# Optimization experiments

Hardware: AMD Instinct MI355X
Metric: run time of the kernel (lower is better)

The kernel has to match this reference:

```python
import jax, jax.numpy as jnp
import numpy as np

N, S, E = 8, 1024, 768
H = 12
D = E // H  # head_dim = 64
FF = 4 * E
EPS = 1e-5


def setup_inputs() -> dict:
    key = jax.random.key(0)
    ks = jax.random.split(key, 12)
    s = lambda fan_in: 1.0 / np.sqrt(fan_in)
    return {
        "x": jax.random.normal(ks[0], (N, S, E), dtype=jnp.float32),
        "ln1_g": jnp.ones((E,), jnp.float32),
        "ln1_b": jnp.zeros((E,), jnp.float32),
        "ln2_g": jnp.ones((E,), jnp.float32),
        "ln2_b": jnp.zeros((E,), jnp.float32),
        "w_attn": jax.random.normal(ks[1], (E, 3 * E), jnp.float32) * s(E),
        "b_attn": jax.random.normal(ks[2], (3 * E,), jnp.float32) * 0.02,
        "w_proj": jax.random.normal(ks[3], (E, E), jnp.float32) * s(E),
        "b_proj": jax.random.normal(ks[4], (E,), jnp.float32) * 0.02,
        "w_fc": jax.random.normal(ks[5], (E, FF), jnp.float32) * s(E),
        "b_fc": jax.random.normal(ks[6], (FF,), jnp.float32) * 0.02,
        "w_fc2": jax.random.normal(ks[7], (FF, E), jnp.float32) * s(FF),
        "b_fc2": jax.random.normal(ks[8], (E,), jnp.float32) * 0.02,
    }


def _layernorm(x, g, b):
    mu = jnp.mean(x, axis=-1, keepdims=True)
    var = jnp.var(x, axis=-1, keepdims=True)
    return (x - mu) * jax.lax.rsqrt(var + EPS) * g + b


def reference(x, ln1_g, ln1_b, ln2_g, ln2_b, w_attn, b_attn, w_proj, b_proj,
              w_fc, b_fc, w_fc2, b_fc2):
    # --- attention branch (pre-LN) ---
    h = _layernorm(x, ln1_g, ln1_b)
    qkv = h @ w_attn + b_attn                       # [N,S,3E]
    q, k, v = jnp.split(qkv, 3, axis=-1)
    q = q.reshape(N, S, H, D).transpose(0, 2, 1, 3)  # [N,H,S,D]
    k = k.reshape(N, S, H, D).transpose(0, 2, 1, 3)
    v = v.reshape(N, S, H, D).transpose(0, 2, 1, 3)
    attn = jnp.einsum('nhsd,nhtd->nhst', q, k) * (1.0 / np.sqrt(D))
    causal = jnp.tril(jnp.ones((S, S), bool))
    attn = jnp.where(causal, attn, -jnp.inf)
    p = jax.nn.softmax(attn, axis=-1)
    out = jnp.einsum('nhst,nhtd->nhsd', p, v)        # [N,H,S,D]
    out = out.transpose(0, 2, 1, 3).reshape(N, S, E)
    x = x + (out @ w_proj + b_proj)
    # --- MLP branch ---
    h2 = _layernorm(x, ln2_g, ln2_b)
    ff = jax.nn.gelu(h2 @ w_fc + b_fc, approximate=False)  # exact GELU (torch nn.GELU default)
    x = x + (ff @ w_fc2 + b_fc2)
    return x
```

## Files before the change

kernel.cpp:

```cpp
#include <hip/hip_runtime.h>
#include <hip/hip_bf16.h>
#include <stdint.h>

#define S_LEN 1024
#define E_DIM 768
#define H_N   12
#define FF_DIM 3072

typedef __hip_bfloat16 bf16;
using short8  = __attribute__((ext_vector_type(8))) short;
using short4v = __attribute__((ext_vector_type(4))) short;
using f32x4   = __attribute__((ext_vector_type(4))) float;

__device__ __forceinline__ void async_cp16(const void* g, void* l) {
  __builtin_amdgcn_global_load_lds(
      (__attribute__((address_space(1))) void*)(g),
      (__attribute__((address_space(3))) void*)(l), 16, 0, 0);
}

__global__ __launch_bounds__(256) void wcastT(const float* __restrict__ w,
                                              bf16* __restrict__ wt,
                                              int K, int N) {
  __shared__ float t[32][33];
  int bx = blockIdx.x;
  int by = blockIdx.y;
  int x = threadIdx.x & 31;
  int y = threadIdx.x >> 5;
  for (int i = y; i < 32; i += 8)
    t[i][x] = w[(size_t)(by * 32 + i) * N + bx * 32 + x];
  __syncthreads();
  for (int i = y; i < 32; i += 8)
    wt[(size_t)(bx * 32 + i) * K + by * 32 + x] = __float2bfloat16(t[x][i]);
}

__global__ __launch_bounds__(256) void ln_rows(const float* __restrict__ x,
                                               const float* __restrict__ g,
                                               const float* __restrict__ b,
                                               bf16* __restrict__ out) {
  int row = blockIdx.x;
  int tid = threadIdx.x;
  const float* xr = x + (size_t)row * E_DIM;
  float v0 = xr[tid], v1 = xr[tid + 256], v2 = xr[tid + 512];
  float s = v0 + v1 + v2;
  float ss = v0 * v0 + v1 * v1 + v2 * v2;
  for (int o = 32; o > 0; o >>= 1) {
    s  += __shfl_down(s, o);
    ss += __shfl_down(ss, o);
  }
  __shared__ float ps[4], pq[4];
  int wv = tid >> 6;
  if ((tid & 63) == 0) { ps[wv] = s; pq[wv] = ss; }
  __syncthreads();
  s  = ps[0] + ps[1] + ps[2] + ps[3];
  ss = pq[0] + pq[1] + pq[2] + pq[3];
  float mu  = s * (1.0f / E_DIM);
  float var = ss * (1.0f / E_DIM) - mu * mu;
  float rs  = rsqrtf(var + 1e-5f);
  bf16* orow = out + (size_t)row * E_DIM;
  orow[tid]       = __float2bfloat16((v0 - mu) * rs * g[tid]       + b[tid]);
  orow[tid + 256] = __float2bfloat16((v1 - mu) * rs * g[tid + 256] + b[tid + 256]);
  orow[tid + 512] = __float2bfloat16((v2 - mu) * rs * g[tid + 512] + b[tid + 512]);
}

template <int MODE>
__global__ __launch_bounds__(256) void gemm_bt(
    const bf16* __restrict__ A, const bf16* __restrict__ Bt,
    const float* __restrict__ bias, const float* __restrict__ resid,
    float* __restrict__ outf, bf16* __restrict__ ob0, bf16* __restrict__ ob1,
    bf16* __restrict__ ob2, int M, int N, int K) {
  __shared__ bf16 As[2][128 * 64];
  __shared__ bf16 Bs[2][128 * 64];
  int tid = threadIdx.x;
  int wave = tid >> 6, lane = tid & 63;
  int quad = lane >> 4, l16 = lane & 15;
  int gx = N >> 7;
  int flat = blockIdx.x;
  int y8 = flat & 7;
  int q2 = flat >> 3;
  int bx = q2 % gx;
  int by = (q2 / gx) * 8 + y8;
  int m0 = by * 128, n0 = bx * 128;
  int wm = (wave & 1) * 64, wn = (wave >> 1) * 64;
  f32x4 acc[4][4];
  for (int i = 0; i < 4; i++)
    for (int j = 0; j < 4; j++)
      for (int r = 0; r < 4; r++) acc[i][j][r] = 0.f;

  int xs = l16 & 7;
  int srow = tid >> 3;
  int cg = (((tid & 7) ^ (srow & 7)) << 3);
  const bf16* aptr = A  + (size_t)(m0 + srow) * K + cg;
  const bf16* bptr = Bt + (size_t)(n0 + srow) * K + cg;

  int nkb = K >> 6;
  {
    bf16* la = &As[0][0] + tid * 8;
    bf16* lb = &Bs[0][0] + tid * 8;
#pragma unroll
    for (int t = 0; t < 4; ++t) {
      async_cp16(aptr + (size_t)t * 32 * K, la + t * 2048);
      async_cp16(bptr + (size_t)t * 32 * K, lb + t * 2048);
    }
  }
  for (int ik = 0; ik < nkb; ++ik) {
    int cur = ik & 1;
    __syncthreads();
    short8 af[2][4], bfr[2][4];
#pragma unroll
    for (int ks = 0; ks < 2; ks++) {
      int ko = (((ks * 4 + quad) ^ xs) << 3);
      for (int i = 0; i < 4; i++)
        af[ks][i] = *(const short8*)&As[cur][(wm + i * 16 + l16) * 64 + ko];
      for (int j = 0; j < 4; j++)
        bfr[ks][j] = *(const short8*)&Bs[cur][(wn + j * 16 + l16) * 64 + ko];
    }
    if (ik + 1 < nkb) {
      size_t ko = (size_t)(ik + 1) * 64;
      bf16* la = &As[cur ^ 1][0] + tid * 8;
      bf16* lb = &Bs[cur ^ 1][0] + tid * 8;
#pragma unroll
      for (int t = 0; t < 4; ++t) {
        async_cp16(aptr + ko + (size_t)t * 32 * K, la + t * 2048);
        async_cp16(bptr + ko + (size_t)t * 32 * K, lb + t * 2048);
      }
    }
#pragma unroll
    for (int ks = 0; ks < 2; ks++)
      for (int i = 0; i < 4; i++)
        for (int j = 0; j < 4; j++)
          acc[i][j] = __builtin_amdgcn_mfma_f32_16x16x32_bf16(
              bfr[ks][j], af[ks][i], acc[i][j], 0, 0, 0);
  }

  for (int j = 0; j < 4; j++) {
    int colb = n0 + wn + j * 16 + quad * 4;
    f32x4 b4 = *(const f32x4*)&bias[colb];
    for (int i = 0; i < 4; i++) {
      int row = m0 + wm + i * 16 + l16;
      f32x4 v = acc[i][j] + b4;
      if (MODE == 0) {
        int nn = row >> 10, s = row & 1023;
        if (colb < 768) {
          int h = colb >> 6, db = colb & 63;
          short4v pk;
          for (int r = 0; r < 4; r++)
            pk[r] = __builtin_bit_cast(short, __float2bfloat16(v[r] * 0.125f));
          *(short4v*)&ob0[(((size_t)nn * H_N + h) * S_LEN + s) * 64 + db] = pk;
        } else if (colb < 1536) {
          int c = colb - 768;
          size_t nh2 = (size_t)nn * H_N + (c >> 6);
          int d = c & 63;
          short4v pk;
          for (int r = 0; r < 4; r++)
            pk[r] = __builtin_bit_cast(short, __float2bfloat16(v[r]));
          *(short4v*)&ob1[((nh2 * 8 + (d >> 3)) * S_LEN + s) * 8 + (d & 7)] = pk;
        } else {
          int c = colb - 1536;
          size_t nh2 = (size_t)nn * H_N + (c >> 6);
          int d0 = c & 63;
          for (int r = 0; r < 4; r++)
            ob2[((nh2 * 128 + (s >> 3)) * 64 + d0 + r) * 8 + (s & 7)] =
                __float2bfloat16(v[r]);
        }
      } else if (MODE == 2) {
        short4v pk;
        for (int r = 0; r < 4; r++) {
          float x = v[r];
          float t = x * (1.59576912161f + 0.0713548162726f * x * x);
          float g = x * __builtin_amdgcn_rcpf(1.0f + __expf(-t));
          pk[r] = __builtin_bit_cast(short, __float2bfloat16(g));
        }
        *(short4v*)&ob0[(size_t)row * N + colb] = pk;
      }
    }
  }
}

__global__ __launch_bounds__(256) void gemm_bt64(
    const bf16* __restrict__ A, const bf16* __restrict__ Bt,
    const float* __restrict__ bias, const float* __restrict__ resid,
    float* __restrict__ outf, int M, int N, int K) {
  __shared__ bf16 As[2][128 * 64];
  __shared__ bf16 Bs[2][64 * 64];
  int tid = threadIdx.x;
  int wave = tid >> 6, lane = tid & 63;
  int quad = lane >> 4, l16 = lane & 15;
  int gx = N >> 6;
  int flat = blockIdx.x;
  int y8 = flat & 7;
  int q2 = flat >> 3;
  int bx = q2 % gx;
  int by = (q2 / gx) * 8 + y8;
  int m0 = by * 128, n0 = bx * 64;
  int wm = wave * 32;
  f32x4 acc[2][4];
  for (int i = 0; i < 2; i++)
    for (int j = 0; j < 4; j++)
      for (int r = 0; r < 4; r++) acc[i][j][r] = 0.f;

  int xs = l16 & 7;
  int srow = tid >> 3;
  int cg = (((tid & 7) ^ (srow & 7)) << 3);
  const bf16* aptr = A  + (size_t)(m0 + srow) * K + cg;
  const bf16* bptr = Bt + (size_t)(n0 + srow) * K + cg;

  int nkb = K >> 6;
  {
    bf16* la = &As[0][0] + tid * 8;
    bf16* lb = &Bs[0][0] + tid * 8;
#pragma unroll
    for (int t = 0; t < 4; ++t)
      async_cp16(aptr + (size_t)t * 32 * K, la + t * 2048);
#pragma unroll
    for (int t = 0; t < 2; ++t)
      async_cp16(bptr + (size_t)t * 32 * K, lb + t * 2048);
  }
  for (int ik = 0; ik < nkb; ++ik) {
    int cur = ik & 1;
    __syncthreads();
    short8 af[2][2], bfr[2][4];
#pragma unroll
    for (int ks = 0; ks < 2; ks++) {
      int ko = (((ks * 4 + quad) ^ xs) << 3);
      for (int i = 0; i < 2; i++)
        af[ks][i] = *(const short8*)&As[cur][(wm + i * 16 + l16) * 64 + ko];
      for (int j = 0; j < 4; j++)
        bfr[ks][j] = *(const short8*)&Bs[cur][(j * 16 + l16) * 64 + ko];
    }
    if (ik + 1 < nkb) {
      size_t ko = (size_t)(ik + 1) * 64;
      bf16* la = &As[cur ^ 1][0] + tid * 8;
      bf16* lb = &Bs[cur ^ 1][0] + tid * 8;
#pragma unroll
      for (int t = 0; t < 4; ++t)
        async_cp16(aptr + ko + (size_t)t * 32 * K, la + t * 2048);
#pragma unroll
      for (int t = 0; t < 2; ++t)
        async_cp16(bptr + ko + (size_t)t * 32 * K, lb + t * 2048);
    }
#pragma unroll
    for (int ks = 0; ks < 2; ks++)
      for (int i = 0; i < 2; i++)
        for (int j = 0; j < 4; j++)
          acc[i][j] = __builtin_amdgcn_mfma_f32_16x16x32_bf16(
              bfr[ks][j], af[ks][i], acc[i][j], 0, 0, 0);
  }

  for (int j = 0; j < 4; j++) {
    int colb = n0 + j * 16 + quad * 4;
    f32x4 b4 = *(const f32x4*)&bias[colb];
    for (int i = 0; i < 2; i++) {
      int row = m0 + wm + i * 16 + l16;
      size_t idx = (size_t)row * N + colb;
      f32x4 rv = *(const f32x4*)&resid[idx];
      *(f32x4*)&outf[idx] = acc[i][j] + b4 + rv;
    }
  }
}

__global__ __launch_bounds__(256) void attn_fwd(
    const bf16* __restrict__ q, const bf16* __restrict__ kg,
    const bf16* __restrict__ vg, bf16* __restrict__ out) {
  __shared__ bf16 kt2[2][8 * 64 * 8];
  __shared__ bf16 vt2[2][8 * 64 * 8];
  __shared__ bf16 pba[4][16 * 68];
  __shared__ bf16 pbb[4][16 * 68];
  int flat = blockIdx.x;
  int xcd = flat & 7;
  int j = flat >> 3;
  int a = j & 7;
  int g = j >> 3;
  int nh = xcd * 12 + g;
  int b = 15 - a;
  int n = nh / H_N, h = nh % H_N;
  int tid = threadIdx.x, wave = tid >> 6, lane = tid & 63;
  int quad = lane >> 4, l16 = lane & 15;
  const bf16* qp = q  + (size_t)nh * S_LEN * 64;
  const bf16* kp = kg + (size_t)nh * 8 * S_LEN * 8;
  const bf16* vp = vg + (size_t)nh * 128 * 64 * 8;
  int qra = a * 64 + wave * 16;
  int qrb = b * 64 + wave * 16;

  short8 qfa[2], qfb[2];
  qfa[0] = *(const short8*)&qp[(size_t)(qra + l16) * 64 + quad * 8];
  qfa[1] = *(const short8*)&qp[(size_t)(qra + l16) * 64 + 32 + quad * 8];
  qfb[0] = *(const short8*)&qp[(size_t)(qrb + l16) * 64 + quad * 8];
  qfb[1] = *(const short8*)&qp[(size_t)(qrb + l16) * 64 + 32 + quad * 8];

  const bf16* kbase = kp + (((size_t)(tid >> 6) * S_LEN) + (tid & 63)) * 8;
  const bf16* vbase = vp + (((size_t)(tid >> 6) * 64) + (tid & 63)) * 8;

  f32x4 oaa[4], oab[4];
  for (int dt = 0; dt < 4; dt++)
    for (int r = 0; r < 4; r++) { oaa[dt][r] = 0.f; oab[dt][r] = 0.f; }
  float lia = 0.f, lib = 0.f;

  {
    bf16* lk = &kt2[0][0] + tid * 8;
    bf16* lv = &vt2[0][0] + tid * 8;
#pragma unroll
    for (int t = 0; t < 2; ++t) {
      async_cp16(kbase + (size_t)t * 4 * S_LEN * 8, lk + t * 2048);
      async_cp16(vbase + (size_t)t * 2048, lv + t * 2048);
    }
  }

  for (int kb = 0; kb <= b; ++kb) {
    bool act_a = (kb <= a);
    int cur = kb & 1;
    __syncthreads();

    short8 kf[2][4], vf[2][4];
#pragma unroll
    for (int ks = 0; ks < 2; ks++)
      for (int nt = 0; nt < 4; nt++) {
        kf[ks][nt] = *(const short8*)
            &kt2[cur][(size_t)((ks * 4 + quad) * 64 + nt * 16 + l16) * 8];
        vf[ks][nt] = *(const short8*)
            &vt2[cur][(size_t)((ks * 4 + quad) * 64 + nt * 16 + l16) * 8];
      }
    if (kb < b) {
      bf16* lk = &kt2[cur ^ 1][0] + tid * 8;
      bf16* lv = &vt2[cur ^ 1][0] + tid * 8;
      size_t kko = (size_t)(kb + 1) * 512;
      size_t vko = (size_t)(kb + 1) * 4096;
#pragma unroll
      for (int t = 0; t < 2; ++t) {
        async_cp16(kbase + kko + (size_t)t * 4 * S_LEN * 8, lk + t * 2048);
        async_cp16(vbase + vko + (size_t)t * 2048, lv + t * 2048);
      }
    }

    f32x4 sb4[4], sa4[4];
    for (int nt = 0; nt < 4; nt++) {
      for (int r = 0; r < 4; r++) { sb4[nt][r] = -10.f; sa4[nt][r] = -10.f; }
      for (int ks = 0; ks < 2; ks++) {
        sb4[nt] = __builtin_amdgcn_mfma_f32_16x16x32_bf16(kf[ks][nt], qfb[ks],
                                                          sb4[nt], 0, 0, 0);
        if (act_a)
          sa4[nt] = __builtin_amdgcn_mfma_f32_16x16x32_bf16(kf[ks][nt], qfa[ks],
                                                            sa4[nt], 0, 0, 0);
      }
    }
    if (kb == b) {
      int ql = wave * 16 + l16;
      for (int nt = 0; nt < 4; nt++)
        for (int r = 0; r < 4; r++)
          if (nt * 16 + quad * 4 + r > ql) sb4[nt][r] = -INFINITY;
    }
    if (kb == a) {
      int ql = wave * 16 + l16;
      for (int nt = 0; nt < 4; nt++)
        for (int r = 0; r < 4; r++)
          if (nt * 16 + quad * 4 + r > ql) sa4[nt][r] = -INFINITY;
    }

    float rsb = 0.f;
    for (int nt = 0; nt < 4; nt++)
      for (int r = 0; r < 4; r++) {
        float p = __expf(sb4[nt][r]);
        sb4[nt][r] = p;
        rsb += p;
      }
    rsb += __shfl_xor(rsb, 16);
    rsb += __shfl_xor(rsb, 32);
    lib += rsb;
    bf16* pwb = pbb[wave];
    for (int nt = 0; nt < 4; nt++) {
      short4v pk;
      for (int r = 0; r < 4; r++)
        pk[r] = __builtin_bit_cast(short, __float2bfloat16(sb4[nt][r]));
      *(short4v*)&pwb[l16 * 68 + nt * 16 + quad * 4] = pk;
    }
    if (act_a) {
      float rsa = 0.f;
      for (int nt = 0; nt < 4; nt++)
        for (int r = 0; r < 4; r++) {
          float p = __expf(sa4[nt][r]);
          sa4[nt][r] = p;
          rsa += p;
        }
      rsa += __shfl_xor(rsa, 16);
      rsa += __shfl_xor(rsa, 32);
      lia += rsa;
      bf16* pwa = pba[wave];
      for (int nt = 0; nt < 4; nt++) {
        short4v pk;
        for (int r = 0; r < 4; r++)
          pk[r] = __builtin_bit_cast(short, __float2bfloat16(sa4[nt][r]));
        *(short4v*)&pwa[l16 * 68 + nt * 16 + quad * 4] = pk;
      }
    }
    asm volatile("s_waitcnt lgkmcnt(0)" ::: "memory");

    for (int ks = 0; ks < 2; ks++) {
      short8 pfb = *(const short8*)&pbb[wave][l16 * 68 + ks * 32 + quad * 8];
      short8 pfa;
      if (act_a) pfa = *(const short8*)&pba[wave][l16 * 68 + ks * 32 + quad * 8];
      for (int dt = 0; dt < 4; dt++) {
        oab[dt] = __builtin_amdgcn_mfma_f32_16x16x32_bf16(vf[ks][dt], pfb,
                                                          oab[dt], 0, 0, 0);
        if (act_a)
          oaa[dt] = __builtin_amdgcn_mfma_f32_16x16x32_bf16(vf[ks][dt], pfa,
                                                            oaa[dt], 0, 0, 0);
      }
    }
  }

  float inva = 1.0f / lia, invb = 1.0f / lib;
  int ta = n * S_LEN + qra + l16;
  int tb = n * S_LEN + qrb + l16;
  for (int dt = 0; dt < 4; dt++) {
    short4v ova, ovb;
    for (int r = 0; r < 4; r++) {
      ova[r] = __builtin_bit_cast(short, __float2bfloat16(oaa[dt][r] * inva));
      ovb[r] = __builtin_bit_cast(short, __float2bfloat16(oab[dt][r] * invb));
    }
    *(short4v*)&out[(size_t)ta * E_DIM + h * 64 + dt * 16 + quad * 4] = ova;
    *(short4v*)&out[(size_t)tb * E_DIM + h * 64 + dt * 16 + quad * 4] = ovb;
  }
}

extern "C" void kernel_launch(void* const* d_in, const int* in_sizes, int n_in,
                              void* d_out, int out_size, void* d_ws, size_t ws_size,
                              hipStream_t stream) {
  (void)in_sizes; (void)n_in; (void)out_size; (void)ws_size;
  const float* x      = (const float*)d_in[0];
  const float* ln1_g  = (const float*)d_in[1];
  const float* ln1_b  = (const float*)d_in[2];
  const float* ln2_g  = (const float*)d_in[3];
  const float* ln2_b  = (const float*)d_in[4];
  const float* w_attn = (const float*)d_in[5];
  const float* b_attn = (const float*)d_in[6];
  const float* w_proj = (const float*)d_in[7];
  const float* b_proj = (const float*)d_in[8];
  const float* w_fc   = (const float*)d_in[9];
  const float* b_fc   = (const float*)d_in[10];
  const float* w_fc2  = (const float*)d_in[11];
  const float* b_fc2  = (const float*)d_in[12];
  float* out = (float*)d_out;

  char* ws = (char*)d_ws;
  bf16* wt_attn = (bf16*)(ws);
  bf16* wt_proj = (bf16*)(ws + 3538944);
  bf16* wt_fc   = (bf16*)(ws + 4718592);
  bf16* wt_fc2  = (bf16*)(ws + 9437184);
  bf16* hbuf    = (bf16*)(ws + 14155776);
  float* x2     = (float*)(ws + 26738688);
  bf16* qb      = (bf16*)(ws + 51904512);
  bf16* kbuf    = (bf16*)(ws + 64487424);
  bf16* vtb     = (bf16*)(ws + 77070336);
  bf16* ao      = (bf16*)(ws + 89653248);
  bf16* ff      = qb;

  dim3 blk(256);
  wcastT<<<dim3(2304 / 32, 768 / 32), blk, 0, stream>>>(w_attn, wt_attn, 768, 2304);
  wcastT<<<dim3(768 / 32, 768 / 32), blk, 0, stream>>>(w_proj, wt_proj, 768, 768);
  wcastT<<<dim3(3072 / 32, 768 / 32), blk, 0, stream>>>(w_fc, wt_fc, 768, 3072);
  wcastT<<<dim3(768 / 32, 3072 / 32), blk, 0, stream>>>(w_fc2, wt_fc2, 3072, 768);

  ln_rows<<<8192, blk, 0, stream>>>(x, ln1_g, ln1_b, hbuf);

  gemm_bt<0><<<dim3(18 * 64), blk, 0, stream>>>(
      hbuf, wt_attn, b_attn, nullptr, nullptr, qb, kbuf, vtb, 8192, 2304, 768);

  attn_fwd<<<dim3(768), blk, 0, stream>>>(qb, kbuf, vtb, ao);

  gemm_bt64<<<dim3(12 * 64), blk, 0, stream>>>(
      ao, wt_proj, b_proj, x, x2, 8192, 768, 768);

  ln_rows<<<8192, blk, 0, stream>>>(x2, ln2_g, ln2_b, hbuf);

  gemm_bt<2><<<dim3(24 * 64), blk, 0, stream>>>(
      hbuf, wt_fc, b_fc, nullptr, nullptr, ff, nullptr, nullptr, 8192, 3072, 768);

  gemm_bt64<<<dim3(12 * 64), blk, 0, stream>>>(
      ff, wt_fc2, b_fc2, x2, out, 8192, 768, 3072);
}
```

Before: 367.9 us.

## Replace async LDS double buffering with register prefetch in GEMMs; merge weight casts

New measurement: 340.8 us. 1.08x faster.

```diff
diff --git a/kernel.cpp b/kernel.cpp
--- a/kernel.cpp
+++ b/kernel.cpp
@@ -18,12 +18,18 @@
       (__attribute__((address_space(3))) void*)(l), 16, 0, 0);
 }
 
-__global__ __launch_bounds__(256) void wcastT(const float* __restrict__ w,
-                                              bf16* __restrict__ wt,
-                                              int K, int N) {
+__global__ __launch_bounds__(256) void wcastT_all(
+    const float* __restrict__ wa, const float* __restrict__ wp,
+    const float* __restrict__ wf, const float* __restrict__ wf2,
+    bf16* __restrict__ oa, bf16* __restrict__ op,
+    bf16* __restrict__ of, bf16* __restrict__ of2) {
   __shared__ float t[32][33];
-  int bx = blockIdx.x;
-  int by = blockIdx.y;
+  int bid = blockIdx.x;
+  const float* w; bf16* wt; int K, N, bx, by;
+  if (bid < 1728)      { w = wa;  wt = oa;  K = 768;  N = 2304; int r = bid;        bx = r % 72; by = r / 72; }
+  else if (bid < 2304) { w = wp;  wt = op;  K = 768;  N = 768;  int r = bid - 1728; bx = r % 24; by = r / 24; }
+  else if (bid < 4608) { w = wf;  wt = of;  K = 768;  N = 3072; int r = bid - 2304; bx = r % 96; by = r / 96; }
+  else                 { w = wf2; wt = of2; K = 3072; N = 768;  int r = bid - 4608; bx = r % 24; by = r / 24; }
   int x = threadIdx.x & 31;
   int y = threadIdx.x >> 5;
   for (int i = y; i < 32; i += 8)
@@ -68,8 +74,8 @@
     const float* __restrict__ bias, const float* __restrict__ resid,
     float* __restrict__ outf, bf16* __restrict__ ob0, bf16* __restrict__ ob1,
     bf16* __restrict__ ob2, int M, int N, int K) {
-  __shared__ bf16 As[2][128 * 64];
-  __shared__ bf16 Bs[2][128 * 64];
+  __shared__ bf16 As[128 * 64];
+  __shared__ bf16 Bs[128 * 64];
   int tid = threadIdx.x;
   int wave = tid >> 6, lane = tid & 63;
   int quad = lane >> 4, l16 = lane & 15;
@@ -88,48 +94,47 @@
 
   int xs = l16 & 7;
   int srow = tid >> 3;
-  int cg = (((tid & 7) ^ (srow & 7)) << 3);
-  const bf16* aptr = A  + (size_t)(m0 + srow) * K + cg;
-  const bf16* bptr = Bt + (size_t)(n0 + srow) * K + cg;
-
+  int scg = (((tid & 7) ^ (srow & 7)) << 3);
+  const bf16* aptr = A  + (size_t)(m0 + srow) * K + scg;
+  const bf16* bptr = Bt + (size_t)(n0 + srow) * K + scg;
+  int ldst = srow * 64 + (tid & 7) * 8;
+
+  short8 pa[4], pb[4];
+#pragma unroll
+  for (int t = 0; t < 4; t++) {
+    pa[t] = *(const short8*)(aptr + (size_t)t * 32 * K);
+    pb[t] = *(const short8*)(bptr + (size_t)t * 32 * K);
+  }
   int nkb = K >> 6;
-  {
-    bf16* la = &As[0][0] + tid * 8;
-    bf16* lb = &Bs[0][0] + tid * 8;
-#pragma unroll
-    for (int t = 0; t < 4; ++t) {
-      async_cp16(aptr + (size_t)t * 32 * K, la + t * 2048);
-      async_cp16(bptr + (size_t)t * 32 * K, lb + t * 2048);
-    }
-  }
   for (int ik = 0; ik < nkb; ++ik) {
-    int cur = ik & 1;
     __syncthreads();
-    short8 af[2][4], bfr[2][4];
-#pragma unroll
-    for (int ks = 0; ks < 2; ks++) {
-      int ko = (((ks * 4 + quad) ^ xs) << 3);
-      for (int i = 0; i < 4; i++)
-        af[ks][i] = *(const short8*)&As[cur][(wm + i * 16 + l16) * 64 + ko];
-      for (int j = 0; j < 4; j++)
-        bfr[ks][j] = *(const short8*)&Bs[cur][(wn + j * 16 + l16) * 64 + ko];
-    }
+#pragma unroll
+    for (int t = 0; t < 4; t++) {
+      *(short8*)&As[ldst + t * 2048] = pa[t];
+      *(short8*)&Bs[ldst + t * 2048] = pb[t];
+    }
+    __syncthreads();
     if (ik + 1 < nkb) {
       size_t ko = (size_t)(ik + 1) * 64;
-      bf16* la = &As[cur ^ 1][0] + tid * 8;
-      bf16* lb = &Bs[cur ^ 1][0] + tid * 8;
-#pragma unroll
-      for (int t = 0; t < 4; ++t) {
-        async_cp16(aptr + ko + (size_t)t * 32 * K, la + t * 2048);
-        async_cp16(bptr + ko + (size_t)t * 32 * K, lb + t * 2048);
-      }
-    }
-#pragma unroll
-    for (int ks = 0; ks < 2; ks++)
+#pragma unroll
+      for (int t = 0; t < 4; t++) {
+        pa[t] = *(const short8*)(aptr + ko + (size_t)t * 32 * K);
+        pb[t] = *(const short8*)(bptr + ko + (size_t)t * 32 * K);
+      }
+    }
+#pragma unroll
+    for (int ks = 0; ks < 2; ks++) {
+      int ko2 = (((ks * 4 + quad) ^ xs) << 3);
+      short8 af[4], bfr[4];
+      for (int i = 0; i < 4; i++)
+        af[i] = *(const short8*)&As[(wm + i * 16 + l16) * 64 + ko2];
+      for (int j = 0; j < 4; j++)
+        bfr[j] = *(const short8*)&Bs[(wn + j * 16 + l16) * 64 + ko2];
       for (int i = 0; i < 4; i++)
         for (int j = 0; j < 4; j++)
           acc[i][j] = __builtin_amdgcn_mfma_f32_16x16x32_bf16(
-              bfr[ks][j], af[ks][i], acc[i][j], 0, 0, 0);
+              bfr[j], af[i], acc[i][j], 0, 0, 0);
+    }
   }
 
   for (int j = 0; j < 4; j++) {
@@ -180,8 +185,8 @@
     const bf16* __restrict__ A, const bf16* __restrict__ Bt,
     const float* __restrict__ bias, const float* __restrict__ resid,
     float* __restrict__ outf, int M, int N, int K) {
-  __shared__ bf16 As[2][128 * 64];
-  __shared__ bf16 Bs[2][64 * 64];
+  __shared__ bf16 As[128 * 64];
+  __shared__ bf16 Bs[64 * 64];
   int tid = threadIdx.x;
   int wave = tid >> 6, lane = tid & 63;
   int quad = lane >> 4, l16 = lane & 15;
@@ -200,50 +205,51 @@
 
   int xs = l16 & 7;
   int srow = tid >> 3;
-  int cg = (((tid & 7) ^ (srow & 7)) << 3);
-  const bf16* aptr = A  + (size_t)(m0 + srow) * K + cg;
-  const bf16* bptr = Bt + (size_t)(n0 + srow) * K + cg;
+  int scg = (((tid & 7) ^ (srow & 7)) << 3);
+  const bf16* aptr = A  + (size_t)(m0 + srow) * K + scg;
+  const bf16* bptr = Bt + (size_t)(n0 + srow) * K + scg;
+  int ldst = srow * 64 + (tid & 7) * 8;
+
+  short8 pa[4], pb[2];
+#pragma unroll
+  for (int t = 0; t < 4; t++)
+    pa[t] = *(const short8*)(aptr + (size_t)t * 32 * K);
+#pragma unroll
+  for (int t = 0; t < 2; t++)
+    pb[t] = *(const short8*)(bptr + (size_t)t * 32 * K);
 
   int nkb = K >> 6;
-  {
-    bf16* la = &As[0][0] + tid * 8;
-    bf16* lb = &Bs[0][0] + tid * 8;
-#pragma unroll
-    for (int t = 0; t < 4; ++t)
-      async_cp16(aptr + (size_t)t * 32 * K, la + t * 2048);
-#pragma unroll
-    for (int t = 0; t < 2; ++t)
-      async_cp16(bptr + (size_t)t * 32 * K, lb + t * 2048);
-  }
   for (int ik = 0; ik < nkb; ++ik) {
-    int cur = ik & 1;
     __syncthreads();
-    short8 af[2][2], bfr[2][4];
-#pragma unroll
-    for (int ks = 0; ks < 2; ks++) {
-      int ko = (((ks * 4 + quad) ^ xs) << 3);
-      for (int i = 0; i < 2; i++)
-        af[ks][i] = *(const short8*)&As[cur][(wm + i * 16 + l16) * 64 + ko];
-      for (int j = 0; j < 4; j++)
-        bfr[ks][j] = *(const short8*)&Bs[cur][(j * 16 + l16) * 64 + ko];
-    }
+#pragma unroll
+    for (int t = 0; t < 4; t++)
+      *(short8*)&As[ldst + t * 2048] = pa[t];
+#pragma unroll
+    for (int t = 0; t < 2; t++)
+      *(short8*)&Bs[ldst + t * 2048] = pb[t];
+    __syncthreads();
     if (ik + 1 < nkb) {
       size_t ko = (size_t)(ik + 1) * 64;
-      bf16* la = &As[cur ^ 1][0] + tid * 8;
-      bf16* lb = &Bs[cur ^ 1][0] + tid * 8;
-#pragma unroll
-      for (int t = 0; t < 4; ++t)
-        async_cp16(aptr + ko + (size_t)t * 32 * K, la + t * 2048);
-#pragma unroll
-      for (int t = 0; t < 2; ++t)
-        async_cp16(bptr + ko + (size_t)t * 32 * K, lb + t * 2048);
-    }
-#pragma unroll
-    for (int ks = 0; ks < 2; ks++)
+#pragma unroll
+      for (int t = 0; t < 4; t++)
+        pa[t] = *(const short8*)(aptr + ko + (size_t)t * 32 * K);
+#pragma unroll
+      for (int t = 0; t < 2; t++)
+        pb[t] = *(const short8*)(bptr + ko + (size_t)t * 32 * K);
+    }
+#pragma unroll
+    for (int ks = 0; ks < 2; ks++) {
+      int ko2 = (((ks * 4 + quad) ^ xs) << 3);
+      short8 af[2], bfr[4];
+      for (int i = 0; i < 2; i++)
+        af[i] = *(const short8*)&As[(wm + i * 16 + l16) * 64 + ko2];
+      for (int j = 0; j < 4; j++)
+        bfr[j] = *(const short8*)&Bs[(j * 16 + l16) * 64 + ko2];
       for (int i = 0; i < 2; i++)
         for (int j = 0; j < 4; j++)
           acc[i][j] = __builtin_amdgcn_mfma_f32_16x16x32_bf16(
-              bfr[ks][j], af[ks][i], acc[i][j], 0, 0, 0);
+              bfr[j], af[i], acc[i][j], 0, 0, 0);
+    }
   }
 
   for (int j = 0; j < 4; j++) {
@@ -454,10 +460,8 @@
   bf16* ff      = qb;
 
   dim3 blk(256);
-  wcastT<<<dim3(2304 / 32, 768 / 32), blk, 0, stream>>>(w_attn, wt_attn, 768, 2304);
-  wcastT<<<dim3(768 / 32, 768 / 32), blk, 0, stream>>>(w_proj, wt_proj, 768, 768);
-  wcastT<<<dim3(3072 / 32, 768 / 32), blk, 0, stream>>>(w_fc, wt_fc, 768, 3072);
-  wcastT<<<dim3(768 / 32, 3072 / 32), blk, 0, stream>>>(w_fc2, wt_fc2, 3072, 768);
+  wcastT_all<<<dim3(6912), blk, 0, stream>>>(w_attn, w_proj, w_fc, w_fc2,
+                                             wt_attn, wt_proj, wt_fc, wt_fc2);
 
   ln_rows<<<8192, blk, 0, stream>>>(x, ln1_g, ln1_b, hbuf);
 
```
